# Kernel tuning notes

Measured on AMD Instinct MI355X. Metric: run time of the kernel, lower is better.

The kernel has to match this reference:

```python
import jax, jax.numpy as jnp
import numpy as np

N_NODES = 50000
N_EDGES = 1_600_000
IN_FEAT = 128
OUT_FEAT = 128
NUM_RELS = 8


def setup_inputs() -> dict:
    key = jax.random.key(0)
    k_h, k_src, k_dst, k_et, k_nrm, k_w, k_b = jax.random.split(key, 7)
    h = jax.random.normal(k_h, (N_NODES, IN_FEAT), dtype=jnp.float32)
    src = jax.random.randint(k_src, (N_EDGES,), 0, N_NODES, dtype=jnp.int32)
    dst = jax.random.randint(k_dst, (N_EDGES,), 0, N_NODES, dtype=jnp.int32)
    etype = jax.random.randint(k_et, (N_EDGES,), 0, NUM_RELS, dtype=jnp.int32)
    norm = jax.random.uniform(k_nrm, (N_EDGES, 1), dtype=jnp.float32)
    W = jax.random.normal(k_w, (NUM_RELS, IN_FEAT, OUT_FEAT), dtype=jnp.float32)
    b = jax.random.normal(k_b, (NUM_RELS, OUT_FEAT), dtype=jnp.float32)
    return {"h": h, "src": src, "dst": dst, "etype": etype, "norm": norm, "W": W, "b": b}


def reference(h, src, dst, etype, norm, W, b):
    # Per-relation node transforms: [R, N, out]. Same math as the DGL code
    # (which computes src_h @ W for all relations then gathers the right one
    # per edge), but computed once per node instead of once per edge.
    H = jnp.einsum('ni,rio->rno', h, W)
    # Gather per-edge transformed message, add per-relation bias, scale by norm.
    msg = (H[etype, src] + b[etype]) * norm  # [E, out]
    # Sum-reduce messages into destination nodes.
    out = jax.ops.segment_sum(msg, dst, num_segments=h.shape[0])  # [N, out]
    return jax.nn.relu(out)
```

## Files before the change

kernel.cpp:

```cpp
#include <hip/hip_runtime.h>

#define N_NODES_C   50000
#define N_EDGES_C   1600000
#define FEAT        128
#define NREL        8
#define NBUCKETS    400000
#define KTOT        1024
#define TILE        16

#define WS_COUNTS   0
#define WS_OFFSETS  400000
#define WS_RANK     2000016
#define WS_BSUM     3600016
#define WS_BOFF     3602064
#define WS_SORTED   3604112
#define WS_HB       10004112
#define WS_WT       22804112
#define WS_NEEDED   23066256

typedef __attribute__((ext_vector_type(8))) short bf16x8;
typedef __attribute__((ext_vector_type(4))) float f32x4;

__device__ __forceinline__ unsigned short f2bf(float f) {
    unsigned u = __float_as_uint(f);
    return (unsigned short)((u + 0x7fffu + ((u >> 16) & 1u)) >> 16);
}
__device__ __forceinline__ float bf2f(unsigned short b) {
    return __uint_as_float((unsigned)b << 16);
}
__device__ __forceinline__ float lo16(unsigned u) { return __uint_as_float(u << 16); }
__device__ __forceinline__ float hi16(unsigned u) { return __uint_as_float(u & 0xffff0000u); }

__global__ void k_prep(const float* __restrict__ h, const float* __restrict__ W,
                       unsigned* __restrict__ counts, unsigned short* __restrict__ hb,
                       unsigned short* __restrict__ wt) {
    int b = blockIdx.x, t = threadIdx.x;
    if (b < 3125) {
        int i = (b * 256 + t) * 8;
        float4 v0 = *(const float4*)&h[i];
        float4 v1 = *(const float4*)&h[i + 4];
        uint4 o;
        o.x = (unsigned)f2bf(v0.x) | ((unsigned)f2bf(v0.y) << 16);
        o.y = (unsigned)f2bf(v0.z) | ((unsigned)f2bf(v0.w) << 16);
        o.z = (unsigned)f2bf(v1.x) | ((unsigned)f2bf(v1.y) << 16);
        o.w = (unsigned)f2bf(v1.z) | ((unsigned)f2bf(v1.w) << 16);
        *(uint4*)&hb[i] = o;
    } else if (b < 3125 + 98) {
        int i = (b - 3125) * 256 + t;
        if (i < 25000) ((uint4*)counts)[i] = make_uint4(0u, 0u, 0u, 0u);
    } else {
        int i = (b - 3223) * 256 + t;
        int n = i >> 10, rk = i & 1023;
        wt[i] = f2bf(W[rk * FEAT + n]);
    }
}

__global__ void k_hist(const int* __restrict__ dst, const int* __restrict__ et,
                       unsigned* __restrict__ counts, unsigned char* __restrict__ rank) {
    int e = blockIdx.x * 256 + threadIdx.x;
    if (e < N_EDGES_C) {
        int key = dst[e] * NREL + et[e];
        int sh = 8 * (key & 3);
        unsigned old = atomicAdd(&counts[key >> 2], 1u << sh);
        rank[e] = (unsigned char)((old >> sh) & 0xffu);
    }
}

__global__ void k_scan_a(const unsigned* __restrict__ counts, unsigned* __restrict__ bsum) {
    __shared__ unsigned s[1024];
    int t = threadIdx.x;
    int i = blockIdx.x * 1024 + t;
    unsigned v = 0;
    if (i < NBUCKETS) v = (counts[i >> 2] >> (8 * (i & 3))) & 0xffu;
    s[t] = v;
    __syncthreads();
    for (int o = 512; o > 0; o >>= 1) {
        if (t < o) s[t] += s[t + o];
        __syncthreads();
    }
    if (t == 0) bsum[blockIdx.x] = s[0];
}

__global__ void k_scan_b(const unsigned* __restrict__ bsum, unsigned* __restrict__ boff, int nb) {
    __shared__ unsigned s[512];
    int t = threadIdx.x;
    unsigned v = (t < nb) ? bsum[t] : 0u;
    s[t] = v;
    __syncthreads();
    for (int o = 1; o < 512; o <<= 1) {
        unsigned u = (t >= o) ? s[t - o] : 0u;
        __syncthreads();
        s[t] += u;
        __syncthreads();
    }
    if (t < nb) boff[t] = s[t] - v;
}

__global__ void k_scan_c(const unsigned* __restrict__ counts, const unsigned* __restrict__ boff,
                         unsigned* __restrict__ offsets) {
    __shared__ unsigned s[1024];
    int t = threadIdx.x;
    int i = blockIdx.x * 1024 + t;
    unsigned v = 0;
    if (i < NBUCKETS) v = (counts[i >> 2] >> (8 * (i & 3))) & 0xffu;
    s[t] = v;
    __syncthreads();
    for (int o = 1; o < 1024; o <<= 1) {
        unsigned u = (t >= o) ? s[t - o] : 0u;
        __syncthreads();
        s[t] += u;
        __syncthreads();
    }
    if (i < NBUCKETS) offsets[i] = boff[blockIdx.x] + s[t] - v;
    if (i == NBUCKETS) offsets[i] = N_EDGES_C;
}

__global__ void k_scatter(const int* __restrict__ src, const int* __restrict__ dst,
                          const int* __restrict__ et, const float* __restrict__ norm,
                          const unsigned* __restrict__ offsets,
                          const unsigned char* __restrict__ rank,
                          unsigned* __restrict__ sorted) {
    int e = blockIdx.x * 256 + threadIdx.x;
    if (e < N_EDGES_C) {
        int key = dst[e] * NREL + et[e];
        unsigned pos = offsets[key] + (unsigned)rank[e];
        sorted[pos] = ((unsigned)src[e] << 16) | (unsigned)f2bf(norm[e]);
    }
}

__global__ __launch_bounds__(512) void k_fused(const unsigned* __restrict__ sorted,
                                               const unsigned* __restrict__ offsets,
                                               const unsigned short* __restrict__ hb,
                                               const unsigned short* __restrict__ wt,
                                               const float* __restrict__ bias,
                                               float* __restrict__ out) {
    __shared__ char At[32768];
    __shared__ float csLds[TILE][NREL];
    int t = threadIdx.x, w = t >> 6, lane = t & 63;
    int node0 = blockIdx.x * TILE;
    int grp = lane >> 4, ln16 = lane & 15;
    int row0 = 2 * w, row1 = 2 * w + 1;

    unsigned bnds0 = offsets[(node0 + row0) * NREL + (lane <= 8 ? lane : 8)];
    unsigned bnds1 = offsets[(node0 + row1) * NREL + (lane <= 8 ? lane : 8)];

#define FLUSH(ROW, J, A0, A1, CS)                                                  \
    do {                                                                           \
        *(unsigned*)(At + (ROW) * 2048 +                                           \
                     (((J) * 256 + lane * 4) ^ (((ROW) & 7) << 4))) =              \
            (unsigned)f2bf(A0) | ((unsigned)f2bf(A1) << 16);                       \
        if (lane == 0) csLds[ROW][J] = (CS);                                       \
    } while (0)

    unsigned p0 = __shfl(bnds0, 0), p1 = __shfl(bnds1, 0);
    int j0 = 0, j1 = 0;
    unsigned bend0 = __shfl(bnds0, 1), bend1 = __shfl(bnds1, 1);
    while (j0 < 8 && p0 >= bend0) {
        FLUSH(row0, j0, 0.f, 0.f, 0.f);
        j0++; if (j0 < 8) bend0 = __shfl(bnds0, j0 + 1);
    }
    while (j1 < 8 && p1 >= bend1) {
        FLUSH(row1, j1, 0.f, 0.f, 0.f);
        j1++; if (j1 < 8) bend1 = __shfl(bnds1, j1 + 1);
    }
    bool live0 = (j0 < 8), live1 = (j1 < 8);
    unsigned rec0 = sorted[live0 ? p0 : 0];
    unsigned rec1 = sorted[live1 ? p1 : 0];
    float a00 = 0.f, a01 = 0.f, cs0 = 0.f;
    float a10 = 0.f, a11 = 0.f, cs1 = 0.f;

    while (live0 | live1) {
        if (live0) {
            unsigned rc = rec0;
            p0++;
            rec0 = sorted[p0 < N_EDGES_C ? p0 : (N_EDGES_C - 1)];
            float nv = bf2f((unsigned short)(rc & 0xffffu));
            unsigned hv = *(const unsigned*)&hb[(size_t)(rc >> 16) * FEAT + lane * 2];
            a00 += nv * lo16(hv);
            a01 += nv * hi16(hv);
            cs0 += nv;
            if (p0 >= bend0) {
                FLUSH(row0, j0, a00, a01, cs0);
                a00 = a01 = cs0 = 0.f;
                j0++; if (j0 < 8) bend0 = __shfl(bnds0, j0 + 1);
                while (j0 < 8 && p0 >= bend0) {
                    FLUSH(row0, j0, 0.f, 0.f, 0.f);
                    j0++; if (j0 < 8) bend0 = __shfl(bnds0, j0 + 1);
                }
                live0 = (j0 < 8);
            }
        }
        if (live1) {
            unsigned rc = rec1;
            p1++;
            rec1 = sorted[p1 < N_EDGES_C ? p1 : (N_EDGES_C - 1)];
            float nv = bf2f((unsigned short)(rc & 0xffffu));
            unsigned hv = *(const unsigned*)&hb[(size_t)(rc >> 16) * FEAT + lane * 2];
            a10 += nv * lo16(hv);
            a11 += nv * hi16(hv);
            cs1 += nv;
            if (p1 >= bend1) {
                FLUSH(row1, j1, a10, a11, cs1);
                a10 = a11 = cs1 = 0.f;
                j1++; if (j1 < 8) bend1 = __shfl(bnds1, j1 + 1);
                while (j1 < 8 && p1 >= bend1) {
                    FLUSH(row1, j1, 0.f, 0.f, 0.f);
                    j1++; if (j1 < 8) bend1 = __shfl(bnds1, j1 + 1);
                }
                live1 = (j1 < 8);
            }
        }
    }
#undef FLUSH
    __syncthreads();

    f32x4 acc = (f32x4){0.f, 0.f, 0.f, 0.f};
    const unsigned short* wcol = wt + (size_t)(w * 16 + ln16) * KTOT + grp * 8;
#pragma unroll 8
    for (int ks = 0; ks < 32; ks++) {
        bf16x8 af = *(const bf16x8*)(At + ln16 * 2048 +
                                     ((ks * 64 + grp * 16) ^ ((ln16 & 7) << 4)));
        bf16x8 bf = *(const bf16x8*)(wcol + ks * 32);
        acc = __builtin_amdgcn_mfma_f32_16x16x32_bf16(af, bf, acc, 0, 0, 0);
    }

#pragma unroll
    for (int i = 0; i < 4; i++) {
        int rl = grp * 4 + i;
        int g  = node0 + rl;
        int col = w * 16 + ln16;
        float v = acc[i];
#pragma unroll
        for (int rr = 0; rr < NREL; rr++) v += csLds[rl][rr] * bias[rr * FEAT + col];
        out[(size_t)g * FEAT + col] = fmaxf(v, 0.f);
    }
}

extern "C" void kernel_launch(void* const* d_in, const int* in_sizes, int n_in,
                              void* d_out, int out_size, void* d_ws, size_t ws_size,
                              hipStream_t stream) {
    const float* h    = (const float*)d_in[0];
    const int*   src  = (const int*)d_in[1];
    const int*   dst  = (const int*)d_in[2];
    const int*   et   = (const int*)d_in[3];
    const float* norm = (const float*)d_in[4];
    const float* W    = (const float*)d_in[5];
    const float* b    = (const float*)d_in[6];
    float*       out  = (float*)d_out;

    if (ws_size < (size_t)WS_NEEDED) return;

    char* ws = (char*)d_ws;
    unsigned*       counts  = (unsigned*)(ws + WS_COUNTS);
    unsigned*       offsets = (unsigned*)(ws + WS_OFFSETS);
    unsigned char*  rank    = (unsigned char*)(ws + WS_RANK);
    unsigned*       bsum    = (unsigned*)(ws + WS_BSUM);
    unsigned*       boff    = (unsigned*)(ws + WS_BOFF);
    unsigned*       sorted  = (unsigned*)(ws + WS_SORTED);
    unsigned short* hb      = (unsigned short*)(ws + WS_HB);
    unsigned short* wt      = (unsigned short*)(ws + WS_WT);

    int nb = (NBUCKETS + 1023) / 1024;

    k_prep<<<3125 + 98 + 512, 256, 0, stream>>>(h, W, counts, hb, wt);
    k_hist<<<6250, 256, 0, stream>>>(dst, et, counts, rank);
    k_scan_a<<<nb, 1024, 0, stream>>>(counts, bsum);
    k_scan_b<<<1, 512, 0, stream>>>(bsum, boff, nb);
    k_scan_c<<<nb, 1024, 0, stream>>>(counts, boff, offsets);
    k_scatter<<<6250, 256, 0, stream>>>(src, dst, et, norm, offsets, rank, sorted);

    k_fused<<<N_NODES_C / TILE, 512, 0, stream>>>(sorted, offsets, hb, wt, b, out);
}
```

Measured before the change: 316.2 us.

## Unroll edge gather by eight with prefetched records over merged two-row segments

The aggregation loop now treats each wave's two destination nodes as one continuous span of 16 (node, relation) segments instead of two interleaved walkers. It batches eight edge records at a time, issues eight independent feature-row gathers together, and prefetches the next eight records, which raises memory-level parallelism over the old one-edge-at-a-time dependent loads. Segment boundaries are handled inside the unrolled loop with a flush loop. The cost is more registers and extra branching for boundary checks.

New measurement: 265.4 us. -16.1%, faster.

```diff
diff --git a/kernel.cpp b/kernel.cpp
--- a/kernel.cpp
+++ b/kernel.cpp
@@ -139,79 +139,67 @@
     int t = threadIdx.x, w = t >> 6, lane = t & 63;
     int node0 = blockIdx.x * TILE;
     int grp = lane >> 4, ln16 = lane & 15;
-    int row0 = 2 * w, row1 = 2 * w + 1;
-
-    unsigned bnds0 = offsets[(node0 + row0) * NREL + (lane <= 8 ? lane : 8)];
-    unsigned bnds1 = offsets[(node0 + row1) * NREL + (lane <= 8 ? lane : 8)];
-
-#define FLUSH(ROW, J, A0, A1, CS)                                                  \
-    do {                                                                           \
-        *(unsigned*)(At + (ROW) * 2048 +                                           \
-                     (((J) * 256 + lane * 4) ^ (((ROW) & 7) << 4))) =              \
-            (unsigned)f2bf(A0) | ((unsigned)f2bf(A1) << 16);                       \
-        if (lane == 0) csLds[ROW][J] = (CS);                                       \
+
+    int kbase = (node0 + 2 * w) * NREL;
+    unsigned bnds = offsets[kbase + (lane <= 16 ? lane : 16)];
+    unsigned pp   = __shfl(bnds, 0);
+    unsigned send = __shfl(bnds, 16);
+    int j = 0;
+    unsigned bend = __shfl(bnds, 1);
+    float a0 = 0.f, a1 = 0.f, cs = 0.f;
+
+#define FLUSHJ(JJ, A0, A1, CS)                                                 \
+    do {                                                                       \
+        int row_ = 2 * w + ((JJ) >> 3);                                        \
+        int jr_  = (JJ) & 7;                                                   \
+        *(unsigned*)(At + row_ * 2048 +                                        \
+                     ((jr_ * 256 + lane * 4) ^ ((row_ & 7) << 4))) =           \
+            (unsigned)f2bf(A0) | ((unsigned)f2bf(A1) << 16);                   \
+        if (lane == 0) csLds[row_][jr_] = (CS);                                \
     } while (0)
 
-    unsigned p0 = __shfl(bnds0, 0), p1 = __shfl(bnds1, 0);
-    int j0 = 0, j1 = 0;
-    unsigned bend0 = __shfl(bnds0, 1), bend1 = __shfl(bnds1, 1);
-    while (j0 < 8 && p0 >= bend0) {
-        FLUSH(row0, j0, 0.f, 0.f, 0.f);
-        j0++; if (j0 < 8) bend0 = __shfl(bnds0, j0 + 1);
-    }
-    while (j1 < 8 && p1 >= bend1) {
-        FLUSH(row1, j1, 0.f, 0.f, 0.f);
-        j1++; if (j1 < 8) bend1 = __shfl(bnds1, j1 + 1);
-    }
-    bool live0 = (j0 < 8), live1 = (j1 < 8);
-    unsigned rec0 = sorted[live0 ? p0 : 0];
-    unsigned rec1 = sorted[live1 ? p1 : 0];
-    float a00 = 0.f, a01 = 0.f, cs0 = 0.f;
-    float a10 = 0.f, a11 = 0.f, cs1 = 0.f;
-
-    while (live0 | live1) {
-        if (live0) {
-            unsigned rc = rec0;
-            p0++;
-            rec0 = sorted[p0 < N_EDGES_C ? p0 : (N_EDGES_C - 1)];
-            float nv = bf2f((unsigned short)(rc & 0xffffu));
-            unsigned hv = *(const unsigned*)&hb[(size_t)(rc >> 16) * FEAT + lane * 2];
-            a00 += nv * lo16(hv);
-            a01 += nv * hi16(hv);
-            cs0 += nv;
-            if (p0 >= bend0) {
-                FLUSH(row0, j0, a00, a01, cs0);
-                a00 = a01 = cs0 = 0.f;
-                j0++; if (j0 < 8) bend0 = __shfl(bnds0, j0 + 1);
-                while (j0 < 8 && p0 >= bend0) {
-                    FLUSH(row0, j0, 0.f, 0.f, 0.f);
-                    j0++; if (j0 < 8) bend0 = __shfl(bnds0, j0 + 1);
-                }
-                live0 = (j0 < 8);
+    unsigned rec[8];
+#pragma unroll
+    for (int u = 0; u < 8; u++) {
+        unsigned q = pp + u;
+        rec[u] = sorted[q < N_EDGES_C ? q : (N_EDGES_C - 1)];
+    }
+
+    while (pp < send) {
+        unsigned hv[8];
+#pragma unroll
+        for (int u = 0; u < 8; u++)
+            hv[u] = *(const unsigned*)&hb[(size_t)(rec[u] >> 16) * FEAT + lane * 2];
+        unsigned nrec[8];
+#pragma unroll
+        for (int u = 0; u < 8; u++) {
+            unsigned q = pp + 8 + u;
+            nrec[u] = sorted[q < N_EDGES_C ? q : (N_EDGES_C - 1)];
+        }
+#pragma unroll
+        for (int u = 0; u < 8; u++) {
+            if (pp >= send) break;
+            while (pp >= bend) {
+                FLUSHJ(j, a0, a1, cs);
+                a0 = a1 = cs = 0.f;
+                j++;
+                bend = __shfl(bnds, j + 1 <= 16 ? j + 1 : 16);
             }
+            float nv = bf2f((unsigned short)(rec[u] & 0xffffu));
+            a0 += nv * lo16(hv[u]);
+            a1 += nv * hi16(hv[u]);
+            cs += nv;
+            pp++;
         }
-        if (live1) {
-            unsigned rc = rec1;
-            p1++;
-            rec1 = sorted[p1 < N_EDGES_C ? p1 : (N_EDGES_C - 1)];
-            float nv = bf2f((unsigned short)(rc & 0xffffu));
-            unsigned hv = *(const unsigned*)&hb[(size_t)(rc >> 16) * FEAT + lane * 2];
-            a10 += nv * lo16(hv);
-            a11 += nv * hi16(hv);
-            cs1 += nv;
-            if (p1 >= bend1) {
-                FLUSH(row1, j1, a10, a11, cs1);
-                a10 = a11 = cs1 = 0.f;
-                j1++; if (j1 < 8) bend1 = __shfl(bnds1, j1 + 1);
-                while (j1 < 8 && p1 >= bend1) {
-                    FLUSH(row1, j1, 0.f, 0.f, 0.f);
-                    j1++; if (j1 < 8) bend1 = __shfl(bnds1, j1 + 1);
-                }
-                live1 = (j1 < 8);
-            }
-        }
-    }
-#undef FLUSH
+#pragma unroll
+        for (int u = 0; u < 8; u++) rec[u] = nrec[u];
+    }
+    while (j < 16) {
+        FLUSHJ(j, a0, a1, cs);
+        a0 = a1 = cs = 0.f;
+        j++;
+    }
+#undef FLUSHJ
     __syncthreads();
 
     f32x4 acc = (f32x4){0.f, 0.f, 0.f, 0.f};
```
